# Kernel optimization log

Hardware: AMD Instinct MI355X
Metric: run time of the kernel (lower is better)

Reference implementation:

```python
import jax, jax.numpy as jnp
import numpy as np

TEMPERATURE = 0.1
EPS = 1e-8  # torch F.cosine_similarity denom clamp


def setup_inputs() -> dict:
    key = jax.random.key(0)
    k1, k2, k3 = jax.random.split(key, 3)
    B, M, D, K = 8, 256, 768, 100
    N = B * M
    transformer_outputs = jax.random.normal(k1, (B, M, D), dtype=jnp.float32)
    cnn_targets = jax.random.normal(k2, (B, M, D), dtype=jnp.float32)
    # uniform sampling with replacement over [0, N) excluding self (multinomial on uniform mask)
    r = jax.random.randint(k3, (N, K), 0, N - 1)
    i = jnp.arange(N)[:, None]
    neg_indices = (r + (r >= i)).astype(jnp.int32)
    return {"transformer_outputs": transformer_outputs, "cnn_targets": cnn_targets, "neg_indices": neg_indices}


def reference(transformer_outputs, cnn_targets, neg_indices):
    B, M, D = transformer_outputs.shape
    N = B * M
    preds = transformer_outputs.reshape(N, D)
    targets = cnn_targets.reshape(N, D)
    pn = preds / jnp.clip(jnp.linalg.norm(preds, axis=-1, keepdims=True), EPS)
    tn = targets / jnp.clip(jnp.linalg.norm(targets, axis=-1, keepdims=True), EPS)
    # all pairwise cosine sims [N, N]; positive on the diagonal, negatives gathered by index
    sim = pn @ tn.T
    pos = jnp.diagonal(sim)                                   # [N]
    neg = sim[jnp.arange(N)[:, None], neg_indices]            # [N, K]
    logits = jnp.concatenate([pos[:, None], neg], axis=1) / TEMPERATURE
    # cross-entropy with label 0 for every row
    loss = -jnp.mean(jax.nn.log_softmax(logits, axis=-1)[:, 0])
    return loss
```

## Files before the change

### kernel.cpp

```cpp
#include <hip/hip_runtime.h>
#include <hip/hip_bf16.h>
#include <math.h>

#define NROWS 2048
#define DDIM  768
#define KNEG  100
#define NLOGITS 101
#define MT 7
#define KW 6
#define ROWB 784

typedef __attribute__((ext_vector_type(4))) float floatx4;

static constexpr float TEMP_INV = 10.0f;
static constexpr float EPS_NORM = 1e-8f;

__device__ __forceinline__ unsigned pack_fp8x4(float a, float b, float c, float d) {
    int u = 0;
    u = __builtin_amdgcn_cvt_pk_fp8_f32(a, b, u, false);
    u = __builtin_amdgcn_cvt_pk_fp8_f32(c, d, u, true);
    return (unsigned)u;
}

__global__ __launch_bounds__(256) void cl_prep_kernel(
        const float* __restrict__ targets,
        unsigned char* __restrict__ tn8) {
    const int wave = threadIdx.x >> 6, lane = threadIdx.x & 63;
    const int row = blockIdx.x * 4 + wave;
    const float4* tv = (const float4*)(targets + (size_t)row * DDIM);
    const float4 a0 = tv[2 * lane], a1 = tv[2 * lane + 1], b0 = tv[128 + lane];

    float ss = 0.f;
    ss = fmaf(a0.x, a0.x, ss); ss = fmaf(a0.y, a0.y, ss);
    ss = fmaf(a0.z, a0.z, ss); ss = fmaf(a0.w, a0.w, ss);
    ss = fmaf(a1.x, a1.x, ss); ss = fmaf(a1.y, a1.y, ss);
    ss = fmaf(a1.z, a1.z, ss); ss = fmaf(a1.w, a1.w, ss);
    ss = fmaf(b0.x, b0.x, ss); ss = fmaf(b0.y, b0.y, ss);
    ss = fmaf(b0.z, b0.z, ss); ss = fmaf(b0.w, b0.w, ss);
    #pragma unroll
    for (int off = 32; off > 0; off >>= 1) ss += __shfl_xor(ss, off);
    const float it = 1.0f / fmaxf(sqrtf(ss), EPS_NORM);

    const unsigned u0 = pack_fp8x4(a0.x * it, a0.y * it, a0.z * it, a0.w * it);
    const unsigned u1 = pack_fp8x4(a1.x * it, a1.y * it, a1.z * it, a1.w * it);
    const unsigned u2 = pack_fp8x4(b0.x * it, b0.y * it, b0.z * it, b0.w * it);

    __shared__ __align__(16) unsigned char buf[4][DDIM];
    *(uint2*)(&buf[wave][8 * lane]) = make_uint2(u0, u1);
    *(unsigned*)(&buf[wave][512 + 4 * lane]) = u2;
    __syncthreads();
    if (lane < 48)
        ((uint4*)(tn8 + (size_t)row * DDIM))[lane] = *(const uint4*)(&buf[wave][16 * lane]);
}

__global__ __launch_bounds__(256, 4) void cl_rowloss_kernel(
        const float* __restrict__ preds,
        const unsigned char* __restrict__ tn8,
        const int* __restrict__ neg_idx,
        float* __restrict__ row_loss) {
    const int i = blockIdx.x;
    const int tid = threadIdx.x;
    const int wave = tid >> 6, lane = tid & 63;

    __shared__ __align__(16) unsigned char pn8[DDIM];
    __shared__ __align__(16) unsigned char Ab[2][16 * ROWB];
    __shared__ __align__(16) float parts[4][MT * 16];
    __shared__ int idx_lds[MT * 16];

    if (tid < MT * 16)
        idx_lds[tid] = (tid == 0 || tid > KNEG) ? i : neg_idx[(size_t)i * KNEG + tid - 1];
    __syncthreads();

    if (wave == 0) {
        const float4* pv = (const float4*)(preds + (size_t)i * DDIM);
        const float4 a0 = pv[2 * lane], a1 = pv[2 * lane + 1], b0 = pv[128 + lane];
        float ss = 0.f;
        ss = fmaf(a0.x, a0.x, ss); ss = fmaf(a0.y, a0.y, ss);
        ss = fmaf(a0.z, a0.z, ss); ss = fmaf(a0.w, a0.w, ss);
        ss = fmaf(a1.x, a1.x, ss); ss = fmaf(a1.y, a1.y, ss);
        ss = fmaf(a1.z, a1.z, ss); ss = fmaf(a1.w, a1.w, ss);
        ss = fmaf(b0.x, b0.x, ss); ss = fmaf(b0.y, b0.y, ss);
        ss = fmaf(b0.z, b0.z, ss); ss = fmaf(b0.w, b0.w, ss);
        #pragma unroll
        for (int off = 32; off > 0; off >>= 1) ss += __shfl_xor(ss, off);
        const float inv = 1.0f / fmaxf(sqrtf(ss), EPS_NORM);
        *(uint2*)(&pn8[8 * lane]) = make_uint2(
            pack_fp8x4(a0.x * inv, a0.y * inv, a0.z * inv, a0.w * inv),
            pack_fp8x4(a1.x * inv, a1.y * inv, a1.z * inv, a1.w * inv));
        *(unsigned*)(&pn8[512 + 4 * lane]) =
            pack_fp8x4(b0.x * inv, b0.y * inv, b0.z * inv, b0.w * inv);
    } else {
        #pragma unroll
        for (int it = 0; it < 4; ++it) {
            const int g = (tid - 64) + 192 * it;
            const int r = g / 48, c = g - r * 48;
            const uint4 v = ((const uint4*)(tn8 + (size_t)idx_lds[r] * DDIM))[c];
            *(uint4*)(&Ab[0][r * ROWB + c * 16]) = v;
        }
    }
    __syncthreads();

    const int kb = wave * KW;
    long long bfr[KW];
    #pragma unroll
    for (int kk = 0; kk < KW; ++kk)
        bfr[kk] = *(const long long*)(&pn8[(kb + kk) * 32 + (lane >> 4) * 8]);

    const int abase = (lane & 15) * ROWB + kb * 32 + (lane >> 4) * 8;

    floatx4 acc[MT] = {};
    #pragma unroll
    for (int t = 0; t < MT; ++t) {
        const int cur = t & 1;
        uint4 stg[3]; int dst[3];
        if (t < MT - 1) {
            #pragma unroll
            for (int it = 0; it < 3; ++it) {
                const int g = tid + 256 * it;
                const int r = g / 48, c = g - r * 48;
                stg[it] = ((const uint4*)(tn8 + (size_t)idx_lds[(t + 1) * 16 + r] * DDIM))[c];
                dst[it] = r * ROWB + c * 16;
            }
        }
        #pragma unroll
        for (int kk = 0; kk < KW; ++kk) {
            const long long af = *(const long long*)(&Ab[cur][abase + kk * 32]);
            acc[t] = __builtin_amdgcn_mfma_f32_16x16x32_fp8_fp8(af, bfr[kk],
                                                                acc[t], 0, 0, 0);
        }
        if (t < MT - 1) {
            #pragma unroll
            for (int it = 0; it < 3; ++it)
                *(uint4*)(&Ab[cur ^ 1][dst[it]]) = stg[it];
        }
        __syncthreads();
    }

    if ((lane & 15) == 0) {
        const int rb = (lane >> 4) * 4;
        #pragma unroll
        for (int t = 0; t < MT; ++t)
            *(floatx4*)(&parts[wave][t * 16 + rb]) = acc[t];
    }
    __syncthreads();

    if (wave == 0) {
        const float v0 = (parts[0][lane] + parts[1][lane] +
                          parts[2][lane] + parts[3][lane]) * TEMP_INV;
        float v1 = -INFINITY;
        if (lane <= NLOGITS - 65)
            v1 = (parts[0][64 + lane] + parts[1][64 + lane] +
                  parts[2][64 + lane] + parts[3][64 + lane]) * TEMP_INV;
        const float l0 = __shfl(v0, 0);
        float m = fmaxf(v0, v1);
        #pragma unroll
        for (int off = 32; off > 0; off >>= 1) m = fmaxf(m, __shfl_xor(m, off));
        float e = expf(v0 - m);
        if (lane <= NLOGITS - 65) e += expf(v1 - m);
        #pragma unroll
        for (int off = 32; off > 0; off >>= 1) e += __shfl_xor(e, off);
        if (lane == 0) row_loss[i] = (m + logf(e)) - l0;
    }
}

__global__ void cl_reduce_kernel(const float* __restrict__ row_loss,
                                 float* __restrict__ out) {
    const int tid = threadIdx.x;
    float s = 0.f;
    #pragma unroll
    for (int c = 0; c < 2; ++c) {
        const float4 v = ((const float4*)row_loss)[tid + 256 * c];
        s += (v.x + v.y) + (v.z + v.w);
    }
    #pragma unroll
    for (int off = 32; off > 0; off >>= 1) s += __shfl_down(s, off);
    __shared__ float sw[4];
    const int wave = tid >> 6, lane = tid & 63;
    if (lane == 0) sw[wave] = s;
    __syncthreads();
    if (tid == 0) out[0] = (sw[0] + sw[1] + sw[2] + sw[3]) / (float)NROWS;
}

extern "C" void kernel_launch(void* const* d_in, const int* in_sizes, int n_in,
                              void* d_out, int out_size, void* d_ws, size_t ws_size,
                              hipStream_t stream) {
    const float* preds   = (const float*)d_in[0];
    const float* targets = (const float*)d_in[1];
    const int*   neg_idx = (const int*)d_in[2];
    float* out = (float*)d_out;

    unsigned char* tn8 = (unsigned char*)d_ws;
    float* row_loss = (float*)((char*)d_ws + (size_t)NROWS * DDIM);

    cl_prep_kernel<<<NROWS / 4, 256, 0, stream>>>(targets, tn8);
    cl_rowloss_kernel<<<NROWS, 256, 0, stream>>>(preds, tn8, neg_idx, row_loss);
    cl_reduce_kernel<<<1, 256, 0, stream>>>(row_loss, out);
}
```

Measured before the change: 25.92 us.

## Use direct global-to-LDS loads with XOR swizzle and fuse final reduction

Gathered fp8 target rows now go straight from global memory into LDS through global_load_lds, replacing the register staging. A XOR swizzle replaces the padded row stride to avoid bank conflicts. The separate reduction kernel is removed: the last block, found with an atomic counter that the prep kernel resets, sums the per-row losses. This saves one kernel launch and register traffic, but adds atomics and fences, and correctness depends on the implicit ordering of the direct-to-LDS loads before the barrier.

```diff
diff --git a/kernel.cpp b/kernel.cpp
--- a/kernel.cpp
+++ b/kernel.cpp
@@ -8,7 +8,6 @@
 #define NLOGITS 101
 #define MT 7
 #define KW 6
-#define ROWB 784
 
 typedef __attribute__((ext_vector_type(4))) float floatx4;
 
@@ -24,7 +23,9 @@
 
 __global__ __launch_bounds__(256) void cl_prep_kernel(
         const float* __restrict__ targets,
-        unsigned char* __restrict__ tn8) {
+        unsigned char* __restrict__ tn8,
+        unsigned* __restrict__ counter) {
+    if (blockIdx.x == 0 && threadIdx.x == 0) *counter = 0;
     const int wave = threadIdx.x >> 6, lane = threadIdx.x & 63;
     const int row = blockIdx.x * 4 + wave;
     const float4* tv = (const float4*)(targets + (size_t)row * DDIM);
@@ -57,19 +58,21 @@
         const float* __restrict__ preds,
         const unsigned char* __restrict__ tn8,
         const int* __restrict__ neg_idx,
-        float* __restrict__ row_loss) {
+        float* __restrict__ row_loss,
+        float* __restrict__ out,
+        unsigned* __restrict__ counter) {
     const int i = blockIdx.x;
     const int tid = threadIdx.x;
     const int wave = tid >> 6, lane = tid & 63;
 
+    __shared__ __align__(16) unsigned char Ab[2][16 * DDIM];
     __shared__ __align__(16) unsigned char pn8[DDIM];
-    __shared__ __align__(16) unsigned char Ab[2][16 * ROWB];
     __shared__ __align__(16) float parts[4][MT * 16];
     __shared__ int idx_lds[MT * 16];
+    __shared__ int lastflag;
 
     if (tid < MT * 16)
         idx_lds[tid] = (tid == 0 || tid > KNEG) ? i : neg_idx[(size_t)i * KNEG + tid - 1];
-    __syncthreads();
 
     if (wave == 0) {
         const float4* pv = (const float4*)(preds + (size_t)i * DDIM);
@@ -89,55 +92,52 @@
             pack_fp8x4(a1.x * inv, a1.y * inv, a1.z * inv, a1.w * inv));
         *(unsigned*)(&pn8[512 + 4 * lane]) =
             pack_fp8x4(b0.x * inv, b0.y * inv, b0.z * inv, b0.w * inv);
-    } else {
-        #pragma unroll
-        for (int it = 0; it < 4; ++it) {
-            const int g = (tid - 64) + 192 * it;
+    }
+    __syncthreads();
+
+    auto stage = [&](int t, int buf) {
+        #pragma unroll
+        for (int it = 0; it < 3; ++it) {
+            const int g = wave * 192 + it * 64 + lane;
             const int r = g / 48, c = g - r * 48;
-            const uint4 v = ((const uint4*)(tn8 + (size_t)idx_lds[r] * DDIM))[c];
-            *(uint4*)(&Ab[0][r * ROWB + c * 16]) = v;
+            const unsigned char* src = tn8 + (size_t)idx_lds[t * 16 + r] * DDIM
+                                       + ((c ^ (r & 7)) << 4);
+            __builtin_amdgcn_global_load_lds(
+                (const __attribute__((address_space(1))) void*)src,
+                (__attribute__((address_space(3))) void*)&Ab[buf][(wave * 192 + it * 64) << 4],
+                16, 0, 0);
         }
-    }
-    __syncthreads();
+    };
 
     const int kb = wave * KW;
+    const int q = lane >> 4;
     long long bfr[KW];
     #pragma unroll
     for (int kk = 0; kk < KW; ++kk)
-        bfr[kk] = *(const long long*)(&pn8[(kb + kk) * 32 + (lane >> 4) * 8]);
-
-    const int abase = (lane & 15) * ROWB + kb * 32 + (lane >> 4) * 8;
+        bfr[kk] = *(const long long*)(&pn8[(kb + kk) * 32 + q * 8]);
+
+    const int aoff = (lane & 15) * DDIM + kb * 32 + q * 8;
+    const int axor = (lane & 7) << 4;
+
+    stage(0, 0);
+    __syncthreads();
 
     floatx4 acc[MT] = {};
     #pragma unroll
     for (int t = 0; t < MT; ++t) {
+        if (t < MT - 1) stage(t + 1, (t + 1) & 1);
         const int cur = t & 1;
-        uint4 stg[3]; int dst[3];
-        if (t < MT - 1) {
-            #pragma unroll
-            for (int it = 0; it < 3; ++it) {
-                const int g = tid + 256 * it;
-                const int r = g / 48, c = g - r * 48;
-                stg[it] = ((const uint4*)(tn8 + (size_t)idx_lds[(t + 1) * 16 + r] * DDIM))[c];
-                dst[it] = r * ROWB + c * 16;
-            }
-        }
         #pragma unroll
         for (int kk = 0; kk < KW; ++kk) {
-            const long long af = *(const long long*)(&Ab[cur][abase + kk * 32]);
+            const long long af = *(const long long*)(&Ab[cur][(aoff + kk * 32) ^ axor]);
             acc[t] = __builtin_amdgcn_mfma_f32_16x16x32_fp8_fp8(af, bfr[kk],
                                                                 acc[t], 0, 0, 0);
         }
-        if (t < MT - 1) {
-            #pragma unroll
-            for (int it = 0; it < 3; ++it)
-                *(uint4*)(&Ab[cur ^ 1][dst[it]]) = stg[it];
-        }
         __syncthreads();
     }
 
     if ((lane & 15) == 0) {
-        const int rb = (lane >> 4) * 4;
+        const int rb = q * 4;
         #pragma unroll
         for (int t = 0; t < MT; ++t)
             *(floatx4*)(&parts[wave][t * 16 + rb]) = acc[t];
@@ -159,26 +159,31 @@
         if (lane <= NLOGITS - 65) e += expf(v1 - m);
         #pragma unroll
         for (int off = 32; off > 0; off >>= 1) e += __shfl_xor(e, off);
-        if (lane == 0) row_loss[i] = (m + logf(e)) - l0;
-    }
-}
-
-__global__ void cl_reduce_kernel(const float* __restrict__ row_loss,
-                                 float* __restrict__ out) {
-    const int tid = threadIdx.x;
-    float s = 0.f;
-    #pragma unroll
-    for (int c = 0; c < 2; ++c) {
-        const float4 v = ((const float4*)row_loss)[tid + 256 * c];
-        s += (v.x + v.y) + (v.z + v.w);
-    }
-    #pragma unroll
-    for (int off = 32; off > 0; off >>= 1) s += __shfl_down(s, off);
-    __shared__ float sw[4];
-    const int wave = tid >> 6, lane = tid & 63;
-    if (lane == 0) sw[wave] = s;
-    __syncthreads();
-    if (tid == 0) out[0] = (sw[0] + sw[1] + sw[2] + sw[3]) / (float)NROWS;
+        if (lane == 0)
+            __hip_atomic_store(&row_loss[i], (m + logf(e)) - l0,
+                               __ATOMIC_RELAXED, __HIP_MEMORY_SCOPE_AGENT);
+    }
+
+    if (tid == 0) {
+        __threadfence();
+        lastflag = (atomicAdd(counter, 1u) == NROWS - 1);
+    }
+    __syncthreads();
+    if (lastflag) {
+        __threadfence();
+        float s = 0.f;
+        #pragma unroll
+        for (int c = 0; c < 2; ++c) {
+            const float4 v = ((const float4*)row_loss)[tid + 256 * c];
+            s += (v.x + v.y) + (v.z + v.w);
+        }
+        #pragma unroll
+        for (int off = 32; off > 0; off >>= 1) s += __shfl_down(s, off);
+        __shared__ float sw[4];
+        if ((tid & 63) == 0) sw[tid >> 6] = s;
+        __syncthreads();
+        if (tid == 0) out[0] = (sw[0] + sw[1] + sw[2] + sw[3]) / (float)NROWS;
+    }
 }
 
 extern "C" void kernel_launch(void* const* d_in, const int* in_sizes, int n_in,
@@ -191,8 +196,9 @@
 
     unsigned char* tn8 = (unsigned char*)d_ws;
     float* row_loss = (float*)((char*)d_ws + (size_t)NROWS * DDIM);
-
-    cl_prep_kernel<<<NROWS / 4, 256, 0, stream>>>(targets, tn8);
-    cl_rowloss_kernel<<<NROWS, 256, 0, stream>>>(preds, tn8, neg_idx, row_loss);
-    cl_reduce_kernel<<<1, 256, 0, stream>>>(row_loss, out);
-}
+    unsigned* counter = (unsigned*)(row_loss + NROWS);
+
+    cl_prep_kernel<<<NROWS / 4, 256, 0, stream>>>(targets, tn8, counter);
+    cl_rowloss_kernel<<<NROWS, 256, 0, stream>>>(preds, tn8, neg_idx,
+                                                 row_loss, out, counter);
+}
```

After: 56.87 us. +119.4%, slower.
